# Performance work log

Measured on AMD Instinct MI355X. Metric: run time of the kernel, lower is better.

The kernel has to match this reference:

```python
import jax, jax.numpy as jnp
import numpy as np

N_NODES = 50000
N_EDGES = 800000
IN_DIM = 256
HID = 32
HEADS = 8
OUT_DIM = 16


def gat_layer(x, src, dst, W, att_s, att_d, bias, concat):
    """PyG-style GATConv (eval mode, add_self_loops already applied to src/dst)."""
    N = x.shape[0]
    H, C = att_s.shape
    h = (x @ W).reshape(N, H, C)                       # [N, H, C]
    a_s = jnp.sum(h * att_s, axis=-1)                  # [N, H]
    a_d = jnp.sum(h * att_d, axis=-1)                  # [N, H]
    alpha = jax.nn.leaky_relu(a_s[src] + a_d[dst], negative_slope=0.2)  # [E, H]
    # segment softmax over edges grouped by destination node
    m = jax.ops.segment_max(alpha, dst, num_segments=N)                 # [N, H]
    e = jnp.exp(alpha - m[dst])
    s = jax.ops.segment_sum(e, dst, num_segments=N)
    coef = e / (s[dst] + 1e-16)                                         # [E, H]
    out = jax.ops.segment_sum(coef[:, :, None] * h[src], dst, num_segments=N)  # [N, H, C]
    out = out.reshape(N, H * C) if concat else out.mean(axis=1)
    return out + bias


def setup_inputs() -> dict:
    key = jax.random.key(0)
    ks = jax.random.split(key, 10)
    x = jax.random.normal(ks[0], (N_NODES, IN_DIM), dtype=jnp.float32)
    edge_index = jax.random.randint(ks[1], (2, N_EDGES), 0, N_NODES, dtype=jnp.int32)
    sc = 0.05
    W1 = jax.random.normal(ks[2], (IN_DIM, HEADS * HID), dtype=jnp.float32) * sc
    att_src1 = jax.random.normal(ks[3], (HEADS, HID), dtype=jnp.float32) * sc
    att_dst1 = jax.random.normal(ks[4], (HEADS, HID), dtype=jnp.float32) * sc
    b1 = jnp.zeros((HEADS * HID,), dtype=jnp.float32)
    W2 = jax.random.normal(ks[5], (HEADS * HID, OUT_DIM), dtype=jnp.float32) * sc
    att_src2 = jax.random.normal(ks[6], (1, OUT_DIM), dtype=jnp.float32) * sc
    att_dst2 = jax.random.normal(ks[7], (1, OUT_DIM), dtype=jnp.float32) * sc
    b2 = jnp.zeros((OUT_DIM,), dtype=jnp.float32)
    return {"x": x, "edge_index": edge_index,
            "W1": W1, "att_src1": att_src1, "att_dst1": att_dst1, "b1": b1,
            "W2": W2, "att_src2": att_src2, "att_dst2": att_dst2, "b2": b2}


def reference(x, edge_index, W1, att_src1, att_dst1, b1, W2, att_src2, att_dst2, b2):
    N = x.shape[0]
    loops = jnp.arange(N, dtype=edge_index.dtype)      # GATConv add_self_loops=True
    src = jnp.concatenate([edge_index[0], loops])
    dst = jnp.concatenate([edge_index[1], loops])
    h = jax.nn.elu(gat_layer(x, src, dst, W1, att_src1, att_dst1, b1, concat=True))
    out = gat_layer(h, src, dst, W2, att_src2, att_dst2, b2, concat=False)
    return out
```

## Files before the change

### kernel.cpp

```cpp
#include <hip/hip_runtime.h>

#define N_NODES 50000
#define N_EDGES 800000
#define E_TOT   (N_EDGES + N_NODES)
#define IN_DIM  256
#define HID     32
#define HEADS   8
#define D1      256
#define OUT_DIM 16

#define SCAN_CHUNK 1024
#define SCAN_NB ((N_NODES + SCAN_CHUNK - 1) / SCAN_CHUNK)
#define PREP_NB (N_NODES * IN_DIM / 4 / 256)
#define CNT_NB  ((E_TOT + 255) / 256)

typedef __attribute__((ext_vector_type(8))) short bf16x8;
typedef __attribute__((ext_vector_type(4))) float f32x4;
typedef __attribute__((ext_vector_type(4))) _Float16 half4;
typedef __attribute__((ext_vector_type(8))) _Float16 half8;

__device__ __forceinline__ unsigned short f2bf(float f) {
  unsigned u = __float_as_uint(f);
  return (unsigned short)((u + 0x7FFFu + ((u >> 16) & 1u)) >> 16);
}
__device__ __forceinline__ float bf2f(unsigned short b) {
  return __uint_as_float(((unsigned)b) << 16);
}
__device__ __forceinline__ float lrelu(float a) { return (a > 0.f) ? a : 0.2f * a; }

__global__ void prep_count(const float* __restrict__ x, unsigned short* __restrict__ xh,
                           unsigned short* __restrict__ xl,
                           const float* __restrict__ W, unsigned short* __restrict__ Wth,
                           unsigned short* __restrict__ Wtl,
                           const int* __restrict__ edst, int* __restrict__ deg,
                           int* __restrict__ rank) {
  const int b = blockIdx.x;
  if (b < PREP_NB) {
    int t = b * 256 + threadIdx.x;
    float4 v = ((const float4*)x)[t];
    ushort4 h, l;
    h.x = f2bf(v.x); l.x = f2bf(v.x - bf2f(h.x));
    h.y = f2bf(v.y); l.y = f2bf(v.y - bf2f(h.y));
    h.z = f2bf(v.z); l.z = f2bf(v.z - bf2f(h.z));
    h.w = f2bf(v.w); l.w = f2bf(v.w - bf2f(h.w));
    ((ushort4*)xh)[t] = h;
    ((ushort4*)xl)[t] = l;
    if (t < IN_DIM * D1) {
      int n = t >> 8, k = t & 255;
      float wv = W[k * D1 + n];
      unsigned short hh = f2bf(wv);
      Wth[n * IN_DIM + k] = hh;
      Wtl[n * IN_DIM + k] = f2bf(wv - bf2f(hh));
    }
  } else {
    int e = (b - PREP_NB) * 256 + threadIdx.x;
    if (e >= E_TOT) return;
    int d = (e < N_EDGES) ? edst[e] : (e - N_EDGES);
    rank[e] = atomicAdd(&deg[d], 1);
  }
}

__global__ __launch_bounds__(256) void gemm1_mfma(
    const unsigned short* __restrict__ Ah_g, const unsigned short* __restrict__ Al_g,
    const unsigned short* __restrict__ Bth_g, const unsigned short* __restrict__ Btl_g,
    const float* __restrict__ att_s, const float* __restrict__ att_d,
    _Float16* __restrict__ C, float* __restrict__ as_, float* __restrict__ ad_) {
  __shared__ short Ah[128][40], Al[128][40];
  __shared__ short Bh[128][40], Bl[128][40];
  const int bm = blockIdx.y * 128, bn = blockIdx.x * 128;
  const int tid = threadIdx.x;
  const int wave = tid >> 6, lane = tid & 63;
  const int l15 = lane & 15, l4 = lane >> 4;
  f32x4 acc[8][2] = {};
  const int sr2 = tid >> 1, sc2 = (tid & 1) * 16;
  const bf16x8 zv = {0, 0, 0, 0, 0, 0, 0, 0};
  for (int k0 = 0; k0 < IN_DIM; k0 += 32) {
    int grow = bm + sr2;
    if (grow < N_NODES) {
      const bf16x8* sH = (const bf16x8*)&Ah_g[(size_t)grow * IN_DIM + k0 + sc2];
      const bf16x8* sL = (const bf16x8*)&Al_g[(size_t)grow * IN_DIM + k0 + sc2];
      *(bf16x8*)&Ah[sr2][sc2] = sH[0];
      *(bf16x8*)&Ah[sr2][sc2 + 8] = sH[1];
      *(bf16x8*)&Al[sr2][sc2] = sL[0];
      *(bf16x8*)&Al[sr2][sc2 + 8] = sL[1];
    } else {
      *(bf16x8*)&Ah[sr2][sc2] = zv;
      *(bf16x8*)&Ah[sr2][sc2 + 8] = zv;
      *(bf16x8*)&Al[sr2][sc2] = zv;
      *(bf16x8*)&Al[sr2][sc2 + 8] = zv;
    }
    {
      const bf16x8* sH = (const bf16x8*)&Bth_g[(size_t)(bn + sr2) * IN_DIM + k0 + sc2];
      const bf16x8* sL = (const bf16x8*)&Btl_g[(size_t)(bn + sr2) * IN_DIM + k0 + sc2];
      *(bf16x8*)&Bh[sr2][sc2] = sH[0];
      *(bf16x8*)&Bh[sr2][sc2 + 8] = sH[1];
      *(bf16x8*)&Bl[sr2][sc2] = sL[0];
      *(bf16x8*)&Bl[sr2][sc2 + 8] = sL[1];
    }
    __syncthreads();
    bf16x8 bh0 = *(bf16x8*)&Bh[wave * 32 + l15][l4 * 8];
    bf16x8 bl0 = *(bf16x8*)&Bl[wave * 32 + l15][l4 * 8];
    bf16x8 bh1 = *(bf16x8*)&Bh[wave * 32 + 16 + l15][l4 * 8];
    bf16x8 bl1 = *(bf16x8*)&Bl[wave * 32 + 16 + l15][l4 * 8];
    #pragma unroll
    for (int i = 0; i < 8; i++) {
      bf16x8 ah = *(bf16x8*)&Ah[i * 16 + l15][l4 * 8];
      bf16x8 al = *(bf16x8*)&Al[i * 16 + l15][l4 * 8];
      acc[i][0] = __builtin_amdgcn_mfma_f32_16x16x32_bf16(ah, bh0, acc[i][0], 0, 0, 0);
      acc[i][0] = __builtin_amdgcn_mfma_f32_16x16x32_bf16(ah, bl0, acc[i][0], 0, 0, 0);
      acc[i][0] = __builtin_amdgcn_mfma_f32_16x16x32_bf16(al, bh0, acc[i][0], 0, 0, 0);
      acc[i][1] = __builtin_amdgcn_mfma_f32_16x16x32_bf16(ah, bh1, acc[i][1], 0, 0, 0);
      acc[i][1] = __builtin_amdgcn_mfma_f32_16x16x32_bf16(ah, bl1, acc[i][1], 0, 0, 0);
      acc[i][1] = __builtin_amdgcn_mfma_f32_16x16x32_bf16(al, bh1, acc[i][1], 0, 0, 0);
    }
    __syncthreads();
  }
  const int head = (bn >> 5) + wave;
  const float sA0 = att_s[head * HID + l15];
  const float sA1 = att_s[head * HID + 16 + l15];
  const float dA0 = att_d[head * HID + l15];
  const float dA1 = att_d[head * HID + 16 + l15];
  #pragma unroll
  for (int i = 0; i < 8; i++) {
    #pragma unroll
    for (int cf = 0; cf < 2; cf++) {
      const int ccol = bn + wave * 32 + cf * 16 + l15;
      #pragma unroll
      for (int r = 0; r < 4; r++) {
        int crow = bm + i * 16 + l4 * 4 + r;
        if (crow < N_NODES) C[(size_t)crow * D1 + ccol] = (_Float16)acc[i][cf][r];
      }
    }
    float ps[4], pd[4];
    #pragma unroll
    for (int r = 0; r < 4; r++) {
      ps[r] = acc[i][0][r] * sA0 + acc[i][1][r] * sA1;
      pd[r] = acc[i][0][r] * dA0 + acc[i][1][r] * dA1;
    }
    #pragma unroll
    for (int m = 1; m < 16; m <<= 1) {
      #pragma unroll
      for (int r = 0; r < 4; r++) {
        ps[r] += __shfl_xor(ps[r], m);
        pd[r] += __shfl_xor(pd[r], m);
      }
    }
    if (l15 == 0) {
      #pragma unroll
      for (int r = 0; r < 4; r++) {
        int crow = bm + i * 16 + l4 * 4 + r;
        if (crow < N_NODES) {
          as_[crow * HEADS + head] = ps[r];
          ad_[crow * HEADS + head] = pd[r];
        }
      }
    }
  }
}

__global__ __launch_bounds__(256) void scan_partial(const int* __restrict__ deg,
                                                    int* __restrict__ offs,
                                                    int* __restrict__ part) {
  __shared__ int ts[256];
  const int tid = threadIdx.x;
  const int idx = blockIdx.x * SCAN_CHUNK + tid * 4;
  int4 v = {0, 0, 0, 0};
  if (idx + 3 < N_NODES) {
    v = *(const int4*)(deg + idx);
  } else {
    if (idx + 0 < N_NODES) v.x = deg[idx + 0];
    if (idx + 1 < N_NODES) v.y = deg[idx + 1];
    if (idx + 2 < N_NODES) v.z = deg[idx + 2];
  }
  ts[tid] = v.x + v.y + v.z + v.w;
  __syncthreads();
  for (int st = 1; st < 256; st <<= 1) {
    int t = (tid >= st) ? ts[tid - st] : 0;
    __syncthreads();
    ts[tid] += t;
    __syncthreads();
  }
  if (tid == 255) part[blockIdx.x] = ts[255];
  int o0 = (tid == 0) ? 0 : ts[tid - 1];
  int4 o;
  o.x = o0; o.y = o0 + v.x; o.z = o.y + v.y; o.w = o.z + v.z;
  if (idx + 3 < N_NODES) {
    *(int4*)(offs + idx) = o;
  } else {
    if (idx + 0 < N_NODES) offs[idx + 0] = o.x;
    if (idx + 1 < N_NODES) offs[idx + 1] = o.y;
    if (idx + 2 < N_NODES) offs[idx + 2] = o.z;
  }
}

__global__ __launch_bounds__(256) void scan_apply(int* __restrict__ offs,
                                                  const int* __restrict__ part) {
  __shared__ int sp[SCAN_NB];
  const int tid = threadIdx.x;
  if (tid < SCAN_NB) sp[tid] = part[tid];
  __syncthreads();
  if (tid == 0) {
    int run = 0;
    #pragma unroll 1
    for (int b = 0; b < SCAN_NB; b++) { int v = sp[b]; sp[b] = run; run += v; }
  }
  __syncthreads();
  int t = blockIdx.x * 256 + tid;
  if (t < N_NODES) offs[t] += sp[t >> 10];
}

__global__ void scatter_edges(const int* __restrict__ esrc, const int* __restrict__ edst,
                              const int* __restrict__ offs, const int* __restrict__ rank,
                              int* __restrict__ srcs) {
  int e = blockIdx.x * blockDim.x + threadIdx.x;
  if (e >= E_TOT) return;
  int s = (e < N_EDGES) ? esrc[e] : (e - N_EDGES);
  int d = (e < N_EDGES) ? edst[e] : (e - N_EDGES);
  srcs[offs[d] + rank[e]] = s;
}

__global__ __launch_bounds__(256) void node_aggr1(
    const int* __restrict__ offs, const int* __restrict__ deg,
    const int* __restrict__ srcs,
    const float* __restrict__ as_, const float* __restrict__ ad_,
    const _Float16* __restrict__ h, const float* __restrict__ bias,
    _Float16* __restrict__ out) {
  const int n = blockIdx.x * 4 + (threadIdx.x >> 6);
  const int lane = threadIdx.x & 63;
  const int base = offs[n], dg = deg[n];
  const int hd = lane >> 3;
  const float adn = ad_[n * HEADS + hd];
  const unsigned c0 = lane * 4;
  float4 acc = {0.f, 0.f, 0.f, 0.f};
  float se = 0.f;
  int e = 0;
  for (; e + 8 <= dg; e += 8) {
    int s[8];
    #pragma unroll
    for (int u = 0; u < 8; u++) s[u] = __builtin_amdgcn_readfirstlane(srcs[base + e + u]);
    half4 hv[8];
    #pragma unroll
    for (int u = 0; u < 8; u++) hv[u] = *(const half4*)(h + ((unsigned)s[u] * D1 + c0));
    float ex[8];
    #pragma unroll
    for (int u = 0; u < 8; u++) ex[u] = __expf(lrelu(as_[(unsigned)s[u] * HEADS + hd] + adn));
    #pragma unroll
    for (int u = 0; u < 8; u++) {
      se += ex[u];
      acc.x += ex[u] * (float)hv[u].x; acc.y += ex[u] * (float)hv[u].y;
      acc.z += ex[u] * (float)hv[u].z; acc.w += ex[u] * (float)hv[u].w;
    }
  }
  for (; e + 4 <= dg; e += 4) {
    int s[4];
    #pragma unroll
    for (int u = 0; u < 4; u++) s[u] = __builtin_amdgcn_readfirstlane(srcs[base + e + u]);
    half4 hv[4];
    #pragma unroll
    for (int u = 0; u < 4; u++) hv[u] = *(const half4*)(h + ((unsigned)s[u] * D1 + c0));
    float ex[4];
    #pragma unroll
    for (int u = 0; u < 4; u++) ex[u] = __expf(lrelu(as_[(unsigned)s[u] * HEADS + hd] + adn));
    #pragma unroll
    for (int u = 0; u < 4; u++) {
      se += ex[u];
      acc.x += ex[u] * (float)hv[u].x; acc.y += ex[u] * (float)hv[u].y;
      acc.z += ex[u] * (float)hv[u].z; acc.w += ex[u] * (float)hv[u].w;
    }
  }
  for (; e < dg; e++) {
    int s = __builtin_amdgcn_readfirstlane(srcs[base + e]);
    float ex = __expf(lrelu(as_[(unsigned)s * HEADS + hd] + adn));
    half4 hv = *(const half4*)(h + ((unsigned)s * D1 + c0));
    se += ex;
    acc.x += ex * (float)hv.x; acc.y += ex * (float)hv.y;
    acc.z += ex * (float)hv.z; acc.w += ex * (float)hv.w;
  }
  const float inv = 1.f / (se + 1e-16f);
  float4 bv = *(const float4*)(bias + c0);
  float4 v;
  v.x = acc.x * inv + bv.x; v.y = acc.y * inv + bv.y;
  v.z = acc.z * inv + bv.z; v.w = acc.w * inv + bv.w;
  v.x = (v.x > 0.f) ? v.x : expm1f(v.x);
  v.y = (v.y > 0.f) ? v.y : expm1f(v.y);
  v.z = (v.z > 0.f) ? v.z : expm1f(v.z);
  v.w = (v.w > 0.f) ? v.w : expm1f(v.w);
  half4 ov;
  ov.x = (_Float16)v.x; ov.y = (_Float16)v.y; ov.z = (_Float16)v.z; ov.w = (_Float16)v.w;
  *(half4*)(out + ((unsigned)n * D1 + c0)) = ov;
}

__global__ __launch_bounds__(256) void gemm2_attn2(
    const _Float16* __restrict__ A, const float* __restrict__ B,
    const float* __restrict__ att_s, const float* __restrict__ att_d,
    _Float16* __restrict__ C, float* __restrict__ as_, float* __restrict__ ad_) {
  __shared__ float Bs[D1 * OUT_DIM];
  const int tid = threadIdx.x;
  #pragma unroll
  for (int i = 0; i < D1 * OUT_DIM / 4 / 256; i++)
    ((float4*)Bs)[tid + i * 256] = ((const float4*)B)[tid + i * 256];
  __syncthreads();
  const int t = blockIdx.x * 256 + tid;
  const int n = t >> 4, c = t & 15;
  const _Float16* arow = A + (size_t)n * D1;
  float acc = 0.f;
  #pragma unroll
  for (int k0 = 0; k0 < D1; k0 += 8) {
    half8 av = *(const half8*)&arow[k0];
    #pragma unroll
    for (int j = 0; j < 8; j++) acc += (float)av[j] * Bs[(k0 + j) * OUT_DIM + c];
  }
  C[t] = (_Float16)acc;
  float ps = acc * att_s[c], pd = acc * att_d[c];
  #pragma unroll
  for (int mS = 1; mS < 16; mS <<= 1) {
    ps += __shfl_xor(ps, mS);
    pd += __shfl_xor(pd, mS);
  }
  if (c == 0) { as_[n] = ps; ad_[n] = pd; }
}

__global__ __launch_bounds__(256) void node_aggr2(
    const int* __restrict__ offs, const int* __restrict__ deg,
    const int* __restrict__ srcs,
    const float* __restrict__ as_, const float* __restrict__ ad_,
    const _Float16* __restrict__ g, const float* __restrict__ bias,
    float* __restrict__ out) {
  const int n = blockIdx.x * 4 + (threadIdx.x >> 6);
  const int lane = threadIdx.x & 63;
  const int base = offs[n], dg = deg[n];
  const float adn = ad_[n];
  const int c = lane & 15, grp = lane >> 4;
  float acc = 0.f, se = 0.f;
  int e = grp;
  for (; e + 8 <= dg + grp; e += 8) {
    unsigned s0 = srcs[base + e], s1 = srcs[base + e + 4];
    float e0 = __expf(lrelu(as_[s0] + adn));
    float e1 = __expf(lrelu(as_[s1] + adn));
    float g0 = (float)g[s0 * OUT_DIM + c], g1 = (float)g[s1 * OUT_DIM + c];
    se += e0 + e1;
    acc += e0 * g0 + e1 * g1;
  }
  for (; e < dg; e += 4) {
    unsigned s = srcs[base + e];
    float ex = __expf(lrelu(as_[s] + adn));
    se += ex;
    acc += ex * (float)g[s * OUT_DIM + c];
  }
  acc += __shfl_xor(acc, 16); se += __shfl_xor(se, 16);
  acc += __shfl_xor(acc, 32); se += __shfl_xor(se, 32);
  if (lane < OUT_DIM) out[n * OUT_DIM + c] = acc / (se + 1e-16f) + bias[c];
}

extern "C" void kernel_launch(void* const* d_in, const int* in_sizes, int n_in,
                              void* d_out, int out_size, void* d_ws, size_t ws_size,
                              hipStream_t stream) {
  const float* x      = (const float*)d_in[0];
  const int*   ei     = (const int*)d_in[1];
  const float* W1     = (const float*)d_in[2];
  const float* att_s1 = (const float*)d_in[3];
  const float* att_d1 = (const float*)d_in[4];
  const float* b1     = (const float*)d_in[5];
  const float* W2     = (const float*)d_in[6];
  const float* att_s2 = (const float*)d_in[7];
  const float* att_d2 = (const float*)d_in[8];
  const float* b2     = (const float*)d_in[9];
  float* out = (float*)d_out;
  const int* esrc = ei;
  const int* edst = ei + N_EDGES;

  char* w = (char*)d_ws;
  _Float16* h1f = (_Float16*)w; w += (size_t)N_NODES * D1 * 2;
  char* regB = w;               w += (size_t)N_NODES * D1 * 4;
  unsigned short* x_hi = (unsigned short*)regB;
  unsigned short* x_lo = x_hi + (size_t)N_NODES * IN_DIM;
  _Float16* h2 = (_Float16*)regB;
  unsigned short* W1t_hi = (unsigned short*)w;  w += (size_t)IN_DIM * D1 * 2;
  unsigned short* W1t_lo = (unsigned short*)w;  w += (size_t)IN_DIM * D1 * 2;
  float* as1 = (float*)w;       w += (size_t)N_NODES * HEADS * 4;
  float* ad1 = (float*)w;       w += (size_t)N_NODES * HEADS * 4;
  _Float16* g2 = (_Float16*)w;  w += (size_t)N_NODES * OUT_DIM * 2;
  float* as2 = (float*)w;       w += (size_t)N_NODES * 4;
  float* ad2 = (float*)w;       w += (size_t)N_NODES * 4;
  int* deg   = (int*)w;         w += (size_t)N_NODES * 4;
  int* offs  = (int*)w;         w += (size_t)N_NODES * 4;
  int* part  = (int*)w;         w += (size_t)64 * 4;
  int* rank  = (int*)w;         w += (size_t)E_TOT * 4;
  int* srcs  = (int*)w;         w += (size_t)E_TOT * 4;

  hipMemsetAsync(deg, 0, (size_t)N_NODES * 4, stream);

  prep_count<<<PREP_NB + CNT_NB, 256, 0, stream>>>(
      x, x_hi, x_lo, W1, W1t_hi, W1t_lo, edst, deg, rank);

  scan_partial<<<SCAN_NB, 256, 0, stream>>>(deg, offs, part);
  scan_apply<<<(N_NODES + 255) / 256, 256, 0, stream>>>(offs, part);
  scatter_edges<<<(E_TOT + 255) / 256, 256, 0, stream>>>(esrc, edst, offs, rank, srcs);

  dim3 gg(D1 / 128, (N_NODES + 127) / 128);
  gemm1_mfma<<<gg, 256, 0, stream>>>(x_hi, x_lo, W1t_hi, W1t_lo,
                                     att_s1, att_d1, h1f, as1, ad1);

  node_aggr1<<<N_NODES / 4, 256, 0, stream>>>(offs, deg, srcs, as1, ad1, h1f, b1, h2);

  gemm2_attn2<<<N_NODES * OUT_DIM / 256, 256, 0, stream>>>(
      h2, W2, att_s2, att_d2, g2, as2, ad2);

  node_aggr2<<<N_NODES / 4, 256, 0, stream>>>(offs, deg, srcs, as2, ad2, g2, b2, out);
}
```

Measured before the change: 247.3 us.

## Move edge degree counting from prep kernel into gemm1 launch

The atomic degree counting is taken out of the bf16 split prep kernel and packed into extra leading blocks of the GEMM1 kernel, each block handling 2048 edges. The grid of the GEMM is flattened to 1D so that count blocks and GEMM tiles share one launch. The aim is to overlap the latency-bound atomics with the compute-bound MFMA GEMM rather than with the bandwidth-bound conversion. The count blocks may delay when GEMM tiles get scheduled, and the prep kernel is now one launch with a separate grid.

```diff
diff --git a/kernel.cpp b/kernel.cpp
--- a/kernel.cpp
+++ b/kernel.cpp
@@ -11,8 +11,8 @@
 
 #define SCAN_CHUNK 1024
 #define SCAN_NB ((N_NODES + SCAN_CHUNK - 1) / SCAN_CHUNK)
-#define PREP_NB (N_NODES * IN_DIM / 4 / 256)
-#define CNT_NB  ((E_TOT + 255) / 256)
+#define CNT8_NB ((E_TOT + 2047) / 2048)
+#define G1_NB   ((D1 / 128) * ((N_NODES + 127) / 128))
 
 typedef __attribute__((ext_vector_type(8))) short bf16x8;
 typedef __attribute__((ext_vector_type(4))) float f32x4;
@@ -28,15 +28,12 @@
 }
 __device__ __forceinline__ float lrelu(float a) { return (a > 0.f) ? a : 0.2f * a; }
 
-__global__ void prep_count(const float* __restrict__ x, unsigned short* __restrict__ xh,
-                           unsigned short* __restrict__ xl,
-                           const float* __restrict__ W, unsigned short* __restrict__ Wth,
-                           unsigned short* __restrict__ Wtl,
-                           const int* __restrict__ edst, int* __restrict__ deg,
-                           int* __restrict__ rank) {
-  const int b = blockIdx.x;
-  if (b < PREP_NB) {
-    int t = b * 256 + threadIdx.x;
+__global__ void prep_all(const float* __restrict__ x, unsigned short* __restrict__ xh,
+                         unsigned short* __restrict__ xl,
+                         const float* __restrict__ W, unsigned short* __restrict__ Wth,
+                         unsigned short* __restrict__ Wtl) {
+  int t = blockIdx.x * blockDim.x + threadIdx.x;
+  if (t < N_NODES * IN_DIM / 4) {
     float4 v = ((const float4*)x)[t];
     ushort4 h, l;
     h.x = f2bf(v.x); l.x = f2bf(v.x - bf2f(h.x));
@@ -45,29 +42,39 @@
     h.w = f2bf(v.w); l.w = f2bf(v.w - bf2f(h.w));
     ((ushort4*)xh)[t] = h;
     ((ushort4*)xl)[t] = l;
-    if (t < IN_DIM * D1) {
-      int n = t >> 8, k = t & 255;
-      float wv = W[k * D1 + n];
-      unsigned short hh = f2bf(wv);
-      Wth[n * IN_DIM + k] = hh;
-      Wtl[n * IN_DIM + k] = f2bf(wv - bf2f(hh));
-    }
-  } else {
-    int e = (b - PREP_NB) * 256 + threadIdx.x;
-    if (e >= E_TOT) return;
-    int d = (e < N_EDGES) ? edst[e] : (e - N_EDGES);
-    rank[e] = atomicAdd(&deg[d], 1);
-  }
-}
-
-__global__ __launch_bounds__(256) void gemm1_mfma(
+  }
+  if (t < IN_DIM * D1) {
+    int n = t >> 8, k = t & 255;
+    float v = W[k * D1 + n];
+    unsigned short h = f2bf(v);
+    Wth[n * IN_DIM + k] = h;
+    Wtl[n * IN_DIM + k] = f2bf(v - bf2f(h));
+  }
+}
+
+__global__ __launch_bounds__(256) void gemm1_count(
     const unsigned short* __restrict__ Ah_g, const unsigned short* __restrict__ Al_g,
     const unsigned short* __restrict__ Bth_g, const unsigned short* __restrict__ Btl_g,
     const float* __restrict__ att_s, const float* __restrict__ att_d,
-    _Float16* __restrict__ C, float* __restrict__ as_, float* __restrict__ ad_) {
+    _Float16* __restrict__ C, float* __restrict__ as_, float* __restrict__ ad_,
+    const int* __restrict__ edst, int* __restrict__ deg, int* __restrict__ rank) {
+  const int bid = blockIdx.x;
+  if (bid < CNT8_NB) {
+    const int eb = bid * 2048 + threadIdx.x;
+    #pragma unroll
+    for (int u = 0; u < 8; u++) {
+      int e = eb + u * 256;
+      if (e < E_TOT) {
+        int d = (e < N_EDGES) ? edst[e] : (e - N_EDGES);
+        rank[e] = atomicAdd(&deg[d], 1);
+      }
+    }
+    return;
+  }
   __shared__ short Ah[128][40], Al[128][40];
   __shared__ short Bh[128][40], Bl[128][40];
-  const int bm = blockIdx.y * 128, bn = blockIdx.x * 128;
+  const int gb = bid - CNT8_NB;
+  const int bm = (gb >> 1) * 128, bn = (gb & 1) * 128;
   const int tid = threadIdx.x;
   const int wave = tid >> 6, lane = tid & 63;
   const int l15 = lane & 15, l4 = lane >> 4;
@@ -390,17 +397,16 @@
 
   hipMemsetAsync(deg, 0, (size_t)N_NODES * 4, stream);
 
-  prep_count<<<PREP_NB + CNT_NB, 256, 0, stream>>>(
-      x, x_hi, x_lo, W1, W1t_hi, W1t_lo, edst, deg, rank);
+  prep_all<<<(N_NODES * IN_DIM / 4 + 255) / 256, 256, 0, stream>>>(
+      x, x_hi, x_lo, W1, W1t_hi, W1t_lo);
+
+  gemm1_count<<<CNT8_NB + G1_NB, 256, 0, stream>>>(
+      x_hi, x_lo, W1t_hi, W1t_lo, att_s1, att_d1, h1f, as1, ad1, edst, deg, rank);
 
   scan_partial<<<SCAN_NB, 256, 0, stream>>>(deg, offs, part);
   scan_apply<<<(N_NODES + 255) / 256, 256, 0, stream>>>(offs, part);
   scatter_edges<<<(E_TOT + 255) / 256, 256, 0, stream>>>(esrc, edst, offs, rank, srcs);
 
-  dim3 gg(D1 / 128, (N_NODES + 127) / 128);
-  gemm1_mfma<<<gg, 256, 0, stream>>>(x_hi, x_lo, W1t_hi, W1t_lo,
-                                     att_s1, att_d1, h1f, as1, ad1);
-
   node_aggr1<<<N_NODES / 4, 256, 0, stream>>>(offs, deg, srcs, as1, ad1, h1f, b1, h2);
 
   gemm2_attn2<<<N_NODES * OUT_DIM / 256, 256, 0, stream>>>(
```

Result: faster. 225.3 us (-8.9%).
